# Kernel optimization log

Measured on AMD Instinct MI355X. Metric: run time of the kernel, lower is better.

The kernel has to match this reference:

```python
import jax, jax.numpy as jnp
import numpy as np

B, T, H, W, CIN = 8, 10, 64, 64, 32
F = 64          # filters
KH, KW = 3, 3
G = 4           # num_gate_copies


def _conv(x, k):
    # x: (N,H,W,Cin), k: (kh,kw,Cin,Cout), SAME padding, stride 1
    return jax.lax.conv_general_dilated(
        x, k, window_strides=(1, 1), padding='SAME',
        dimension_numbers=('NHWC', 'HWIO', 'NHWC'))


def setup_inputs() -> dict:
    key = jax.random.key(0)
    k1, k2, k3, k4 = jax.random.split(key, 4)
    inputs = jax.random.normal(k1, (B, T, H, W, CIN), dtype=jnp.float32)
    label_values = jax.random.randint(k2, (B,), 0, G, dtype=jnp.int32)
    kernel = jax.random.normal(k3, (KH, KW, CIN, 4 * F), dtype=jnp.float32) * 0.05
    recurrent_kernel = jax.random.normal(k4, (G, KH, KW, F, 4 * F), dtype=jnp.float32) * 0.05
    # unit_forget_bias: zeros with forget-gate slice set to 1.0
    bias = jnp.zeros((G, 4 * F), dtype=jnp.float32).at[:, F:2 * F].set(1.0)
    return {"inputs": inputs, "label_values": label_values,
            "kernel": kernel, "recurrent_kernel": recurrent_kernel, "bias": bias}


def reference(inputs, label_values, kernel, recurrent_kernel, bias):
    b, t, h_dim, w_dim, _ = inputs.shape
    f = recurrent_kernel.shape[-1] // 4
    # Per-sample gather of expert recurrent kernel / bias (label-indexed)
    k_b = recurrent_kernel[label_values]   # (B, kh, kw, F, 4F)
    b_b = bias[label_values]               # (B, 4F)

    # vmapped per-sample batch=1 recurrent conv (faithful to map_fn semantics)
    per_sample_conv = jax.vmap(lambda hs, ks: _conv(hs[None], ks)[0])

    def step(carry, x_t):
        h, c = carry
        z = _conv(x_t, kernel) + per_sample_conv(h, k_b) + b_b[:, None, None, :]
        i = jax.nn.sigmoid(z[..., :f])
        fg = jax.nn.sigmoid(z[..., f:2 * f])
        g = jnp.tanh(z[..., 2 * f:3 * f])
        o = jax.nn.sigmoid(z[..., 3 * f:])
        c_new = fg * c + i * g
        h_new = o * jnp.tanh(c_new)
        return (h_new, c_new), h_new

    h0 = jnp.zeros((b, h_dim, w_dim, f), dtype=inputs.dtype)
    c0 = jnp.zeros_like(h0)
    xs = jnp.moveaxis(inputs, 1, 0)  # (T, B, H, W, Cin)
    _, ys = jax.lax.scan(step, (h0, c0), xs)
    return jnp.moveaxis(ys, 0, 1)    # (B, T, H, W, F)
```

## Files before the change

### kernel.cpp

```cpp
#include <hip/hip_runtime.h>


typedef __attribute__((ext_vector_type(8))) short short8v;
typedef __attribute__((ext_vector_type(4))) float f32x4;
typedef __attribute__((ext_vector_type(4))) unsigned int u32x4;
typedef unsigned short u16;

__device__ __forceinline__ u16 f2bf(float x) {
    union { float f; unsigned u; } a; a.f = x;
    unsigned r = a.u + 0x7FFFu + ((a.u >> 16) & 1u);
    return (u16)(r >> 16);
}
__device__ __forceinline__ float sigf(float x) { return 1.0f / (1.0f + __expf(-x)); }
__device__ __forceinline__ float tanhf_(float x) {
    float e = __expf(2.0f * x);
    return 1.0f - 2.0f / (e + 1.0f);
}

__global__ __launch_bounds__(256)
void prep_w(const float* __restrict__ kern, const float* __restrict__ rk,
            u16* __restrict__ wt_in, u16* __restrict__ wt_rk,
            unsigned* __restrict__ flags) {
    int idx = blockIdx.x * 256 + threadIdx.x;
    if (blockIdx.x == 0) flags[threadIdx.x] = 0u;
    if (idx >= 82944) return;
    const float* s;
    u16* dst;
    if (idx < 9216) {
        int co = idx & 255, ckb = idx >> 8;
        int tap = ckb >> 2, kb = ckb & 3;
        s = kern + (size_t)((tap << 5) + (kb << 3)) * 256 + co;
        dst = wt_in + (size_t)idx * 8;
    } else {
        int j = idx - 9216;
        int co = j & 255, rest = j >> 8;
        int kb = rest & 3, gc = rest >> 2;
        int g = gc / 18, cc = gc - g * 18;
        int tap = cc >> 1;
        int cib = (cc & 1) << 5;
        s = rk + (size_t)(((g * 9 + tap) << 6) + cib + (kb << 3)) * 256 + co;
        dst = wt_rk + (size_t)j * 8;
    }
    union { u16 u[8]; uint4 q; } o;
    #pragma unroll
    for (int i = 0; i < 8; ++i) o.u[i] = f2bf(s[i * 256]);
    *(uint4*)dst = o.q;
}

__device__ __forceinline__ void stageX(const float* __restrict__ src,
                                       short* __restrict__ halX,
                                       int tid, int y0, int x0) {
    #pragma unroll 2
    for (int s = tid; s < 720; s += 512) {
        int pos = s >> 2, kb = s & 3;
        int hy = pos / 10, hx = pos - hy * 10;
        int gy = y0 + hy - 1, gx = x0 + hx - 1;
        union { u16 u[8]; short8v v; } o;
        o.v = (short8v){0,0,0,0,0,0,0,0};
        if ((unsigned)gy < 64u && (unsigned)gx < 64u) {
            const float* p = src + (((gy << 6) + gx) << 5) + (kb << 3);
            float4 a0 = *(const float4*)p;
            float4 a1 = *(const float4*)(p + 4);
            o.u[0] = f2bf(a0.x); o.u[1] = f2bf(a0.y);
            o.u[2] = f2bf(a0.z); o.u[3] = f2bf(a0.w);
            o.u[4] = f2bf(a1.x); o.u[5] = f2bf(a1.y);
            o.u[6] = f2bf(a1.z); o.u[7] = f2bf(a1.w);
        }
        *(short8v*)&halX[kb * 1440 + pos * 8] = o.v;
    }
}

__global__ __launch_bounds__(512)
void lstm_all(const float* __restrict__ xf,
              const u16* __restrict__ wt_in, const u16* __restrict__ wt_rk,
              const float* __restrict__ bias, const int* __restrict__ labels,
              u16* __restrict__ hb0, u16* __restrict__ hb1,
              float* __restrict__ out, unsigned* __restrict__ flags)
{
    __shared__ short hal[17280];

    const int tid  = threadIdx.x;
    const int lane = tid & 63;
    const int w    = tid >> 6;
    const int pxh  = w >> 2;
    const int wq   = w & 3;
    const int b    = blockIdx.x >> 5;
    const int tile = blockIdx.x & 31;
    const int ty = tile >> 3, tx = tile & 7;
    const int y0 = ty << 4, x0 = tx << 3;
    const int g = labels[b];

    const int co_l = lane & 15;
    const int kbl  = lane >> 4;
    const int prow = (lane & 15) >> 3, pcol = lane & 7;
    const int f = (wq << 4) + co_l;

    float bv[4];
    #pragma unroll
    for (int n = 0; n < 4; ++n)
        bv[n] = bias[(g << 8) + (n << 6) + f];

    int aoffm[4];
    #pragma unroll
    for (int m = 0; m < 4; ++m)
        aoffm[m] = ((pxh << 3) + (m << 1) + prow) * 10 + pcol;

    int poff[4][4];
    #pragma unroll
    for (int m = 0; m < 4; ++m)
        #pragma unroll
        for (int rr = 0; rr < 4; ++rr) {
            int pf = (kbl << 2) + rr;
            int yy = y0 + (pxh << 3) + (m << 1) + (pf >> 3);
            int xx = x0 + (pf & 7);
            poff[m][rr] = (((yy << 6) + xx) << 6) + f;
        }

    float cst[4][4];
    #pragma unroll
    for (int m = 0; m < 4; ++m)
        #pragma unroll
        for (int rr = 0; rr < 4; ++rr) cst[m][rr] = 0.0f;

    const float* xsrc = xf + ((size_t)b * 10 << 17);
    float*       ob0  = out + ((size_t)b * 10 << 18);
    unsigned*    myfl = flags + (b << 5) + tile;

    for (int s = tid; s < 1440; s += 512)
        *(short8v*)&hal[5760 + s * 8] = (short8v){0,0,0,0,0,0,0,0};
    stageX(xsrc, hal, tid, y0, x0);
    __syncthreads();

    for (int t = 0; t < 10; ++t) {
        u16* hw = ((t & 1) ? hb1 : hb0) + ((size_t)b << 18);

        f32x4 acc[4][4];
        #pragma unroll
        for (int n = 0; n < 4; ++n)
            #pragma unroll
            for (int m = 0; m < 4; ++m)
                acc[m][n] = (f32x4){bv[n], bv[n], bv[n], bv[n]};

        #pragma unroll 3
        for (int tap = 0; tap < 9; ++tap) {
            const int koff = (tap / 3) * 10 + (tap % 3);
            const u16* wb = wt_in + (size_t)((((tap << 2) + kbl) << 8) + (wq << 4) + co_l) * 8;
            short8v bfr[4], af[4];
            #pragma unroll
            for (int n = 0; n < 4; ++n)
                bfr[n] = *(const short8v*)&wb[(size_t)n << 9];
            #pragma unroll
            for (int m = 0; m < 4; ++m)
                af[m] = *(const short8v*)&hal[kbl * 1440 + (aoffm[m] + koff) * 8];
            #pragma unroll
            for (int m = 0; m < 4; ++m)
                #pragma unroll
                for (int n = 0; n < 4; ++n)
                    acc[m][n] = __builtin_amdgcn_mfma_f32_16x16x32_bf16(af[m], bfr[n], acc[m][n], 0, 0, 0);
        }
        if (t > 0) {
            #pragma unroll 3
            for (int c = 0; c < 18; ++c) {
                const int tap = c >> 1;
                const int koff = (tap / 3) * 10 + (tap % 3);
                const u16* wb = wt_rk + (size_t)(((((g * 18 + c) << 2) + kbl) << 8) + (wq << 4) + co_l) * 8;
                short8v bfr[4], af[4];
                #pragma unroll
                for (int n = 0; n < 4; ++n)
                    bfr[n] = *(const short8v*)&wb[(size_t)n << 9];
                const int abase = 5760 + (((c & 1) << 2) + kbl) * 1440;
                #pragma unroll
                for (int m = 0; m < 4; ++m)
                    af[m] = *(const short8v*)&hal[abase + (aoffm[m] + koff) * 8];
                #pragma unroll
                for (int m = 0; m < 4; ++m)
                    #pragma unroll
                    for (int n = 0; n < 4; ++n)
                        acc[m][n] = __builtin_amdgcn_mfma_f32_16x16x32_bf16(af[m], bfr[n], acc[m][n], 0, 0, 0);
            }
        }
        __syncthreads();

        float* ob = ob0 + ((size_t)t << 18);
        #pragma unroll
        for (int m = 0; m < 4; ++m) {
            #pragma unroll
            for (int rr = 0; rr < 4; ++rr) {
                float zi = acc[m][0][rr], zf = acc[m][1][rr];
                float zg = acc[m][2][rr], zo = acc[m][3][rr];
                float cn = sigf(zf) * cst[m][rr] + sigf(zi) * tanhf_(zg);
                float hn = sigf(zo) * tanhf_(cn);
                cst[m][rr] = cn;
                ob[poff[m][rr]] = hn;
                int pf = (kbl << 2) + rr;
                int ly = (pxh << 3) + (m << 1) + (pf >> 3);
                int lx = pf & 7;
                hal[5760 + (f >> 3) * 1440 + ((ly + 1) * 10 + lx + 1) * 8 + (f & 7)]
                    = (short)f2bf(hn);
            }
        }
        __syncthreads();

        if (t < 9) {
            if (tid < 352) {
                int pxr = tid >> 3, kb = tid & 7;
                int dy, dx;
                if (pxr < 8)       { dy = 0;  dx = pxr; }
                else if (pxr < 16) { dy = 15; dx = pxr - 8; }
                else { int v = pxr - 16; dy = 1 + (v >> 1); dx = (v & 1) * 7; }
                u32x4 v = *(const u32x4*)&hal[5760 + kb * 1440 + ((dy + 1) * 10 + dx + 1) * 8];
                const u16* ga = hw + ((((y0 + dy) << 6) + x0 + dx) << 6) + (kb << 3);
                asm volatile("global_store_dwordx4 %0, %1, off sc0 sc1"
                             :: "v"(ga), "v"(v) : "memory");
            }
            asm volatile("s_waitcnt vmcnt(0)" ::: "memory");
            __syncthreads();
            if (tid == 0)
                __hip_atomic_fetch_add(myfl, 1u, __ATOMIC_RELAXED,
                                       __HIP_MEMORY_SCOPE_SYSTEM);

            stageX(xsrc + ((size_t)(t + 1) << 17), hal, tid, y0, x0);

            if (tid < 64) {
                int k = tid;
                bool valid = false; int fidx = 0;
                if (k < 8) {
                    int kk = k + (k >= 4);
                    int nty = ty + kk / 3 - 1, ntx = tx + kk % 3 - 1;
                    valid = (unsigned)nty < 4u && (unsigned)ntx < 8u;
                    fidx = (b << 5) + (nty << 3) + ntx;
                }
                unsigned tgt = (unsigned)(t + 1);
                int guard = 0;
                for (;;) {
                    unsigned vv = tgt;
                    if (valid)
                        vv = __hip_atomic_load(flags + fidx, __ATOMIC_RELAXED,
                                               __HIP_MEMORY_SCOPE_SYSTEM);
                    if (__all(vv >= tgt)) break;
                    if (++guard > (1 << 18)) break;
                    __builtin_amdgcn_s_sleep(2);
                }
            }
            __syncthreads();

            if (tid < 416) {
                int posr = tid >> 3, kb = tid & 7;
                int hy, hx;
                if (posr < 10)      { hy = 0;  hx = posr; }
                else if (posr < 20) { hy = 17; hx = posr - 10; }
                else { int v = posr - 20; hy = 1 + (v >> 1); hx = (v & 1) * 9; }
                int gy = y0 + hy - 1, gx = x0 + hx - 1;
                bool inb = (unsigned)gy < 64u && (unsigned)gx < 64u;
                const u16* ga = inb ? (hw + (((gy << 6) + gx) << 6) + (kb << 3)) : hw;
                u32x4 v;
                asm volatile("global_load_dwordx4 %0, %1, off sc0 sc1"
                             : "=v"(v) : "v"(ga) : "memory");
                asm volatile("s_waitcnt vmcnt(0)" ::: "memory");
                __builtin_amdgcn_sched_barrier(0);
                if (!inb) v = (u32x4){0u, 0u, 0u, 0u};
                *(u32x4*)&hal[5760 + kb * 1440 + (hy * 10 + hx) * 8] = v;
            }
            __syncthreads();
        }
    }
}

extern "C" void kernel_launch(void* const* d_in, const int* in_sizes, int n_in,
                              void* d_out, int out_size, void* d_ws, size_t ws_size,
                              hipStream_t stream)
{
    const float* x    = (const float*)d_in[0];
    const int*   lbl  = (const int*)  d_in[1];
    const float* kern = (const float*)d_in[2];
    const float* rk   = (const float*)d_in[3];
    const float* bias = (const float*)d_in[4];
    float* out = (float*)d_out;

    u16* hb0   = (u16*)d_ws;
    u16* hb1   = hb0 + 2097152;
    u16* wt_in = hb1 + 2097152;
    u16* wt_rk = wt_in + 73728;
    unsigned* flags = (unsigned*)(wt_rk + 589824);

    hipLaunchKernelGGL(prep_w, dim3(324), dim3(256), 0, stream,
                       kern, rk, wt_in, wt_rk, flags);

    void* args[] = { (void*)&x, (void*)&wt_in, (void*)&wt_rk, (void*)&bias,
                     (void*)&lbl, (void*)&hb0, (void*)&hb1, (void*)&out,
                     (void*)&flags };
    (void)hipLaunchCooperativeKernel((const void*)lstm_all, dim3(256), dim3(512),
                                     args, 0, stream);
}
```

Baseline: 209.3 us.

## Pre-convert input to bf16, double warps per tile, overlap input conv with halo wait

Result: slower. 236.2 us (+12.9%).

```diff
diff --git a/kernel.cpp b/kernel.cpp
--- a/kernel.cpp
+++ b/kernel.cpp
@@ -15,6 +15,18 @@
 __device__ __forceinline__ float tanhf_(float x) {
     float e = __expf(2.0f * x);
     return 1.0f - 2.0f / (e + 1.0f);
+}
+
+__global__ __launch_bounds__(256)
+void prep_x(const float* __restrict__ x, u16* __restrict__ xb) {
+    size_t i = (size_t)blockIdx.x * 256 + threadIdx.x;
+    for (; i < 2621440u; i += (size_t)2048 * 256) {
+        float4 v = ((const float4*)x)[i];
+        union { u16 u[4]; uint2 q; } o;
+        o.u[0] = f2bf(v.x); o.u[1] = f2bf(v.y);
+        o.u[2] = f2bf(v.z); o.u[3] = f2bf(v.w);
+        ((uint2*)xb)[i] = o.q;
+    }
 }
 
 __global__ __launch_bounds__(256)
@@ -47,31 +59,8 @@
     *(uint4*)dst = o.q;
 }
 
-__device__ __forceinline__ void stageX(const float* __restrict__ src,
-                                       short* __restrict__ halX,
-                                       int tid, int y0, int x0) {
-    #pragma unroll 2
-    for (int s = tid; s < 720; s += 512) {
-        int pos = s >> 2, kb = s & 3;
-        int hy = pos / 10, hx = pos - hy * 10;
-        int gy = y0 + hy - 1, gx = x0 + hx - 1;
-        union { u16 u[8]; short8v v; } o;
-        o.v = (short8v){0,0,0,0,0,0,0,0};
-        if ((unsigned)gy < 64u && (unsigned)gx < 64u) {
-            const float* p = src + (((gy << 6) + gx) << 5) + (kb << 3);
-            float4 a0 = *(const float4*)p;
-            float4 a1 = *(const float4*)(p + 4);
-            o.u[0] = f2bf(a0.x); o.u[1] = f2bf(a0.y);
-            o.u[2] = f2bf(a0.z); o.u[3] = f2bf(a0.w);
-            o.u[4] = f2bf(a1.x); o.u[5] = f2bf(a1.y);
-            o.u[6] = f2bf(a1.z); o.u[7] = f2bf(a1.w);
-        }
-        *(short8v*)&halX[kb * 1440 + pos * 8] = o.v;
-    }
-}
-
-__global__ __launch_bounds__(512)
-void lstm_all(const float* __restrict__ xf,
+__global__ __launch_bounds__(1024)
+void lstm_all(const u16* __restrict__ xb,
               const u16* __restrict__ wt_in, const u16* __restrict__ wt_rk,
               const float* __restrict__ bias, const int* __restrict__ labels,
               u16* __restrict__ hb0, u16* __restrict__ hb1,
@@ -82,7 +71,7 @@
     const int tid  = threadIdx.x;
     const int lane = tid & 63;
     const int w    = tid >> 6;
-    const int pxh  = w >> 2;
+    const int pxq  = w >> 2;
     const int wq   = w & 3;
     const int b    = blockIdx.x >> 5;
     const int tile = blockIdx.x & 31;
@@ -100,103 +89,151 @@
     for (int n = 0; n < 4; ++n)
         bv[n] = bias[(g << 8) + (n << 6) + f];
 
-    int aoffm[4];
-    #pragma unroll
-    for (int m = 0; m < 4; ++m)
-        aoffm[m] = ((pxh << 3) + (m << 1) + prow) * 10 + pcol;
-
-    int poff[4][4];
-    #pragma unroll
-    for (int m = 0; m < 4; ++m)
+    int aoffm[2];
+    #pragma unroll
+    for (int mf = 0; mf < 2; ++mf)
+        aoffm[mf] = ((pxq << 2) + (mf << 1) + prow) * 10 + pcol;
+
+    int poff[2][4], loff[2][4];
+    #pragma unroll
+    for (int mf = 0; mf < 2; ++mf)
         #pragma unroll
         for (int rr = 0; rr < 4; ++rr) {
             int pf = (kbl << 2) + rr;
-            int yy = y0 + (pxh << 3) + (m << 1) + (pf >> 3);
-            int xx = x0 + (pf & 7);
-            poff[m][rr] = (((yy << 6) + xx) << 6) + f;
-        }
-
-    float cst[4][4];
-    #pragma unroll
-    for (int m = 0; m < 4; ++m)
+            int ly = (pxq << 2) + (mf << 1) + (pf >> 3);
+            int lx = pf & 7;
+            poff[mf][rr] = ((((y0 + ly) << 6) + x0 + lx) << 6) + f;
+            loff[mf][rr] = 5760 + (f >> 3) * 1440 + ((ly + 1) * 10 + lx + 1) * 8 + (f & 7);
+        }
+
+    float cst[2][4];
+    #pragma unroll
+    for (int mf = 0; mf < 2; ++mf)
         #pragma unroll
-        for (int rr = 0; rr < 4; ++rr) cst[m][rr] = 0.0f;
-
-    const float* xsrc = xf + ((size_t)b * 10 << 17);
-    float*       ob0  = out + ((size_t)b * 10 << 18);
-    unsigned*    myfl = flags + (b << 5) + tile;
-
-    for (int s = tid; s < 1440; s += 512)
+        for (int rr = 0; rr < 4; ++rr) cst[mf][rr] = 0.0f;
+
+    const u16* xsrc = xb + ((size_t)b * 10 << 17);
+    float*     ob0  = out + ((size_t)b * 10 << 18);
+    unsigned*  myfl = flags + (b << 5) + tile;
+
+    for (int s = tid; s < 1440; s += 1024)
         *(short8v*)&hal[5760 + s * 8] = (short8v){0,0,0,0,0,0,0,0};
-    stageX(xsrc, hal, tid, y0, x0);
+    if (tid < 720) {
+        int pos = tid >> 2, kb = tid & 3;
+        int hy = pos / 10, hx = pos - hy * 10;
+        int gy = y0 + hy - 1, gx = x0 + hx - 1;
+        short8v v = (short8v){0,0,0,0,0,0,0,0};
+        if ((unsigned)gy < 64u && (unsigned)gx < 64u)
+            v = *(const short8v*)&xsrc[(((gy << 6) + gx) << 5) + (kb << 3)];
+        *(short8v*)&hal[kb * 1440 + pos * 8] = v;
+    }
     __syncthreads();
 
     for (int t = 0; t < 10; ++t) {
         u16* hw = ((t & 1) ? hb1 : hb0) + ((size_t)b << 18);
 
-        f32x4 acc[4][4];
+        f32x4 acc[2][4];
         #pragma unroll
         for (int n = 0; n < 4; ++n)
             #pragma unroll
-            for (int m = 0; m < 4; ++m)
-                acc[m][n] = (f32x4){bv[n], bv[n], bv[n], bv[n]};
+            for (int mf = 0; mf < 2; ++mf)
+                acc[mf][n] = (f32x4){bv[n], bv[n], bv[n], bv[n]};
 
         #pragma unroll 3
         for (int tap = 0; tap < 9; ++tap) {
             const int koff = (tap / 3) * 10 + (tap % 3);
-            const u16* wb = wt_in + (size_t)((((tap << 2) + kbl) << 8) + (wq << 4) + co_l) * 8;
-            short8v bfr[4], af[4];
+            const u16* wb = wt_in + (size_t)((((tap << 2) + kbl) << 8) + f) * 8;
+            short8v bfr[4], af[2];
             #pragma unroll
             for (int n = 0; n < 4; ++n)
                 bfr[n] = *(const short8v*)&wb[(size_t)n << 9];
             #pragma unroll
-            for (int m = 0; m < 4; ++m)
-                af[m] = *(const short8v*)&hal[kbl * 1440 + (aoffm[m] + koff) * 8];
-            #pragma unroll
-            for (int m = 0; m < 4; ++m)
+            for (int mf = 0; mf < 2; ++mf)
+                af[mf] = *(const short8v*)&hal[kbl * 1440 + (aoffm[mf] + koff) * 8];
+            #pragma unroll
+            for (int mf = 0; mf < 2; ++mf)
                 #pragma unroll
                 for (int n = 0; n < 4; ++n)
-                    acc[m][n] = __builtin_amdgcn_mfma_f32_16x16x32_bf16(af[m], bfr[n], acc[m][n], 0, 0, 0);
-        }
+                    acc[mf][n] = __builtin_amdgcn_mfma_f32_16x16x32_bf16(af[mf], bfr[n], acc[mf][n], 0, 0, 0);
+        }
+
         if (t > 0) {
+            if (tid < 64) {
+                bool valid = false; int fidx = 0;
+                if (tid < 8) {
+                    int kk = tid + (tid >= 4);
+                    int nty = ty + kk / 3 - 1, ntx = tx + kk % 3 - 1;
+                    valid = (unsigned)nty < 4u && (unsigned)ntx < 8u;
+                    fidx = (b << 5) + (nty << 3) + ntx;
+                }
+                unsigned tgt = (unsigned)t;
+                int guard = 0;
+                for (;;) {
+                    unsigned vv = tgt;
+                    if (valid)
+                        vv = __hip_atomic_load(flags + fidx, __ATOMIC_RELAXED,
+                                               __HIP_MEMORY_SCOPE_SYSTEM);
+                    if (__all(vv >= tgt)) break;
+                    if (++guard > (1 << 18)) break;
+                    __builtin_amdgcn_s_sleep(2);
+                }
+            }
+            __syncthreads();
+
+            if (tid < 416) {
+                const u16* hr = ((t & 1) ? hb0 : hb1) + ((size_t)b << 18);
+                int posr = tid >> 3, kb = tid & 7;
+                int hy, hx;
+                if (posr < 10)      { hy = 0;  hx = posr; }
+                else if (posr < 20) { hy = 17; hx = posr - 10; }
+                else { int v = posr - 20; hy = 1 + (v >> 1); hx = (v & 1) * 9; }
+                int gy = y0 + hy - 1, gx = x0 + hx - 1;
+                bool inb = (unsigned)gy < 64u && (unsigned)gx < 64u;
+                const u16* ga = inb ? (hr + (((gy << 6) + gx) << 6) + (kb << 3)) : hr;
+                u32x4 v;
+                asm volatile("global_load_dwordx4 %0, %1, off sc0 sc1"
+                             : "=v"(v) : "v"(ga) : "memory");
+                asm volatile("s_waitcnt vmcnt(0)" ::: "memory");
+                __builtin_amdgcn_sched_barrier(0);
+                if (!inb) v = (u32x4){0u, 0u, 0u, 0u};
+                *(u32x4*)&hal[5760 + kb * 1440 + (hy * 10 + hx) * 8] = v;
+            }
+            __syncthreads();
+
             #pragma unroll 3
             for (int c = 0; c < 18; ++c) {
                 const int tap = c >> 1;
                 const int koff = (tap / 3) * 10 + (tap % 3);
-                const u16* wb = wt_rk + (size_t)(((((g * 18 + c) << 2) + kbl) << 8) + (wq << 4) + co_l) * 8;
-                short8v bfr[4], af[4];
+                const u16* wb = wt_rk + (size_t)(((((g * 18 + c) << 2) + kbl) << 8) + f) * 8;
+                short8v bfr[4], af[2];
                 #pragma unroll
                 for (int n = 0; n < 4; ++n)
                     bfr[n] = *(const short8v*)&wb[(size_t)n << 9];
                 const int abase = 5760 + (((c & 1) << 2) + kbl) * 1440;
                 #pragma unroll
-                for (int m = 0; m < 4; ++m)
-                    af[m] = *(const short8v*)&hal[abase + (aoffm[m] + koff) * 8];
+                for (int mf = 0; mf < 2; ++mf)
+                    af[mf] = *(const short8v*)&hal[abase + (aoffm[mf] + koff) * 8];
                 #pragma unroll
-                for (int m = 0; m < 4; ++m)
+                for (int mf = 0; mf < 2; ++mf)
                     #pragma unroll
                     for (int n = 0; n < 4; ++n)
-                        acc[m][n] = __builtin_amdgcn_mfma_f32_16x16x32_bf16(af[m], bfr[n], acc[m][n], 0, 0, 0);
+                        acc[mf][n] = __builtin_amdgcn_mfma_f32_16x16x32_bf16(af[mf], bfr[n], acc[mf][n], 0, 0, 0);
             }
         }
         __syncthreads();
 
         float* ob = ob0 + ((size_t)t << 18);
         #pragma unroll
-        for (int m = 0; m < 4; ++m) {
+        for (int mf = 0; mf < 2; ++mf) {
             #pragma unroll
             for (int rr = 0; rr < 4; ++rr) {
-                float zi = acc[m][0][rr], zf = acc[m][1][rr];
-                float zg = acc[m][2][rr], zo = acc[m][3][rr];
-                float cn = sigf(zf) * cst[m][rr] + sigf(zi) * tanhf_(zg);
+                float zi = acc[mf][0][rr], zf = acc[mf][1][rr];
+                float zg = acc[mf][2][rr], zo = acc[mf][3][rr];
+                float cn = sigf(zf) * cst[mf][rr] + sigf(zi) * tanhf_(zg);
                 float hn = sigf(zo) * tanhf_(cn);
-                cst[m][rr] = cn;
-                ob[poff[m][rr]] = hn;
-                int pf = (kbl << 2) + rr;
-                int ly = (pxh << 3) + (m << 1) + (pf >> 3);
-                int lx = pf & 7;
-                hal[5760 + (f >> 3) * 1440 + ((ly + 1) * 10 + lx + 1) * 8 + (f & 7)]
-                    = (short)f2bf(hn);
+                cst[mf][rr] = cn;
+                ob[poff[mf][rr]] = hn;
+                hal[loff[mf][rr]] = (short)f2bf(hn);
             }
         }
         __syncthreads();
@@ -219,47 +256,15 @@
                 __hip_atomic_fetch_add(myfl, 1u, __ATOMIC_RELAXED,
                                        __HIP_MEMORY_SCOPE_SYSTEM);
 
-            stageX(xsrc + ((size_t)(t + 1) << 17), hal, tid, y0, x0);
-
-            if (tid < 64) {
-                int k = tid;
-                bool valid = false; int fidx = 0;
-                if (k < 8) {
-                    int kk = k + (k >= 4);
-                    int nty = ty + kk / 3 - 1, ntx = tx + kk % 3 - 1;
-                    valid = (unsigned)nty < 4u && (unsigned)ntx < 8u;
-                    fidx = (b << 5) + (nty << 3) + ntx;
-                }
-                unsigned tgt = (unsigned)(t + 1);
-                int guard = 0;
-                for (;;) {
-                    unsigned vv = tgt;
-                    if (valid)
-                        vv = __hip_atomic_load(flags + fidx, __ATOMIC_RELAXED,
-                                               __HIP_MEMORY_SCOPE_SYSTEM);
-                    if (__all(vv >= tgt)) break;
-                    if (++guard > (1 << 18)) break;
-                    __builtin_amdgcn_s_sleep(2);
-                }
-            }
-            __syncthreads();
-
-            if (tid < 416) {
-                int posr = tid >> 3, kb = tid & 7;
-                int hy, hx;
-                if (posr < 10)      { hy = 0;  hx = posr; }
-                else if (posr < 20) { hy = 17; hx = posr - 10; }
-                else { int v = posr - 20; hy = 1 + (v >> 1); hx = (v & 1) * 9; }
+            if (tid < 720) {
+                const u16* src = xsrc + ((size_t)(t + 1) << 17);
+                int pos = tid >> 2, kb = tid & 3;
+                int hy = pos / 10, hx = pos - hy * 10;
                 int gy = y0 + hy - 1, gx = x0 + hx - 1;
-                bool inb = (unsigned)gy < 64u && (unsigned)gx < 64u;
-                const u16* ga = inb ? (hw + (((gy << 6) + gx) << 6) + (kb << 3)) : hw;
-                u32x4 v;
-                asm volatile("global_load_dwordx4 %0, %1, off sc0 sc1"
-                             : "=v"(v) : "v"(ga) : "memory");
-                asm volatile("s_waitcnt vmcnt(0)" ::: "memory");
-                __builtin_amdgcn_sched_barrier(0);
-                if (!inb) v = (u32x4){0u, 0u, 0u, 0u};
-                *(u32x4*)&hal[5760 + kb * 1440 + (hy * 10 + hx) * 8] = v;
+                short8v v = (short8v){0,0,0,0,0,0,0,0};
+                if ((unsigned)gy < 64u && (unsigned)gx < 64u)
+                    v = *(const short8v*)&src[(((gy << 6) + gx) << 5) + (kb << 3)];
+                *(short8v*)&hal[kb * 1440 + pos * 8] = v;
             }
             __syncthreads();
         }
@@ -277,18 +282,20 @@
     const float* bias = (const float*)d_in[4];
     float* out = (float*)d_out;
 
-    u16* hb0   = (u16*)d_ws;
+    u16* xb    = (u16*)d_ws;
+    u16* hb0   = xb + 10485760;
     u16* hb1   = hb0 + 2097152;
     u16* wt_in = hb1 + 2097152;
     u16* wt_rk = wt_in + 73728;
     unsigned* flags = (unsigned*)(wt_rk + 589824);
 
+    hipLaunchKernelGGL(prep_x, dim3(2048), dim3(256), 0, stream, x, xb);
     hipLaunchKernelGGL(prep_w, dim3(324), dim3(256), 0, stream,
                        kern, rk, wt_in, wt_rk, flags);
 
-    void* args[] = { (void*)&x, (void*)&wt_in, (void*)&wt_rk, (void*)&bias,
+    void* args[] = { (void*)&xb, (void*)&wt_in, (void*)&wt_rk, (void*)&bias,
                      (void*)&lbl, (void*)&hb0, (void*)&hb1, (void*)&out,
                      (void*)&flags };
-    (void)hipLaunchCooperativeKernel((const void*)lstm_all, dim3(256), dim3(512),
+    (void)hipLaunchCooperativeKernel((const void*)lstm_all, dim3(256), dim3(1024),
                                      args, 0, stream);
 }
```

## Overlap neighbor-flag wait with input conv, pre-convert x to bf16, pad LDS stride

Applied to the files above, without the earlier changes.

After: 201.0 us. -3.9%, faster.

```diff
diff --git a/kernel.cpp b/kernel.cpp
--- a/kernel.cpp
+++ b/kernel.cpp
@@ -6,6 +6,9 @@
 typedef __attribute__((ext_vector_type(4))) unsigned int u32x4;
 typedef unsigned short u16;
 
+#define HS 1448
+#define HB 5760
+
 __device__ __forceinline__ u16 f2bf(float x) {
     union { float f; unsigned u; } a; a.f = x;
     unsigned r = a.u + 0x7FFFu + ((a.u >> 16) & 1u);
@@ -15,6 +18,18 @@
 __device__ __forceinline__ float tanhf_(float x) {
     float e = __expf(2.0f * x);
     return 1.0f - 2.0f / (e + 1.0f);
+}
+
+__global__ __launch_bounds__(256)
+void prep_x(const float* __restrict__ x, u16* __restrict__ xb) {
+    size_t i = (size_t)blockIdx.x * 256 + threadIdx.x;
+    for (; i < 2621440u; i += (size_t)2048 * 256) {
+        float4 v = ((const float4*)x)[i];
+        union { u16 u[4]; uint2 q; } o;
+        o.u[0] = f2bf(v.x); o.u[1] = f2bf(v.y);
+        o.u[2] = f2bf(v.z); o.u[3] = f2bf(v.w);
+        ((uint2*)xb)[i] = o.q;
+    }
 }
 
 __global__ __launch_bounds__(256)
@@ -47,7 +62,7 @@
     *(uint4*)dst = o.q;
 }
 
-__device__ __forceinline__ void stageX(const float* __restrict__ src,
+__device__ __forceinline__ void stageX(const u16* __restrict__ src,
                                        short* __restrict__ halX,
                                        int tid, int y0, int x0) {
     #pragma unroll 2
@@ -55,29 +70,21 @@
         int pos = s >> 2, kb = s & 3;
         int hy = pos / 10, hx = pos - hy * 10;
         int gy = y0 + hy - 1, gx = x0 + hx - 1;
-        union { u16 u[8]; short8v v; } o;
-        o.v = (short8v){0,0,0,0,0,0,0,0};
-        if ((unsigned)gy < 64u && (unsigned)gx < 64u) {
-            const float* p = src + (((gy << 6) + gx) << 5) + (kb << 3);
-            float4 a0 = *(const float4*)p;
-            float4 a1 = *(const float4*)(p + 4);
-            o.u[0] = f2bf(a0.x); o.u[1] = f2bf(a0.y);
-            o.u[2] = f2bf(a0.z); o.u[3] = f2bf(a0.w);
-            o.u[4] = f2bf(a1.x); o.u[5] = f2bf(a1.y);
-            o.u[6] = f2bf(a1.z); o.u[7] = f2bf(a1.w);
-        }
-        *(short8v*)&halX[kb * 1440 + pos * 8] = o.v;
+        short8v v = (short8v){0,0,0,0,0,0,0,0};
+        if ((unsigned)gy < 64u && (unsigned)gx < 64u)
+            v = *(const short8v*)&src[(((gy << 6) + gx) << 5) + (kb << 3)];
+        *(short8v*)&halX[kb * 1440 + pos * 8] = v;
     }
 }
 
 __global__ __launch_bounds__(512)
-void lstm_all(const float* __restrict__ xf,
+void lstm_all(const u16* __restrict__ xb,
               const u16* __restrict__ wt_in, const u16* __restrict__ wt_rk,
               const float* __restrict__ bias, const int* __restrict__ labels,
               u16* __restrict__ hb0, u16* __restrict__ hb1,
               float* __restrict__ out, unsigned* __restrict__ flags)
 {
-    __shared__ short hal[17280];
+    __shared__ short hal[HB + 8 * HS];
 
     const int tid  = threadIdx.x;
     const int lane = tid & 63;
@@ -105,15 +112,16 @@
     for (int m = 0; m < 4; ++m)
         aoffm[m] = ((pxh << 3) + (m << 1) + prow) * 10 + pcol;
 
-    int poff[4][4];
+    int poff[4][4], loff[4][4];
     #pragma unroll
     for (int m = 0; m < 4; ++m)
         #pragma unroll
         for (int rr = 0; rr < 4; ++rr) {
             int pf = (kbl << 2) + rr;
-            int yy = y0 + (pxh << 3) + (m << 1) + (pf >> 3);
-            int xx = x0 + (pf & 7);
-            poff[m][rr] = (((yy << 6) + xx) << 6) + f;
+            int ly = (pxh << 3) + (m << 1) + (pf >> 3);
+            int lx = pf & 7;
+            poff[m][rr] = ((((y0 + ly) << 6) + x0 + lx) << 6) + f;
+            loff[m][rr] = HB + (f >> 3) * HS + ((ly + 1) * 10 + lx + 1) * 8 + (f & 7);
         }
 
     float cst[4][4];
@@ -122,12 +130,12 @@
         #pragma unroll
         for (int rr = 0; rr < 4; ++rr) cst[m][rr] = 0.0f;
 
-    const float* xsrc = xf + ((size_t)b * 10 << 17);
-    float*       ob0  = out + ((size_t)b * 10 << 18);
-    unsigned*    myfl = flags + (b << 5) + tile;
-
-    for (int s = tid; s < 1440; s += 512)
-        *(short8v*)&hal[5760 + s * 8] = (short8v){0,0,0,0,0,0,0,0};
+    const u16* xsrc = xb + ((size_t)b * 10 << 17);
+    float*     ob0  = out + ((size_t)b * 10 << 18);
+    unsigned*  myfl = flags + (b << 5) + tile;
+
+    for (int s = tid; s < 1448; s += 512)
+        *(short8v*)&hal[HB + s * 8] = (short8v){0,0,0,0,0,0,0,0};
     stageX(xsrc, hal, tid, y0, x0);
     __syncthreads();
 
@@ -144,7 +152,7 @@
         #pragma unroll 3
         for (int tap = 0; tap < 9; ++tap) {
             const int koff = (tap / 3) * 10 + (tap % 3);
-            const u16* wb = wt_in + (size_t)((((tap << 2) + kbl) << 8) + (wq << 4) + co_l) * 8;
+            const u16* wb = wt_in + (size_t)((((tap << 2) + kbl) << 8) + f) * 8;
             short8v bfr[4], af[4];
             #pragma unroll
             for (int n = 0; n < 4; ++n)
@@ -158,79 +166,17 @@
                 for (int n = 0; n < 4; ++n)
                     acc[m][n] = __builtin_amdgcn_mfma_f32_16x16x32_bf16(af[m], bfr[n], acc[m][n], 0, 0, 0);
         }
+
         if (t > 0) {
-            #pragma unroll 3
-            for (int c = 0; c < 18; ++c) {
-                const int tap = c >> 1;
-                const int koff = (tap / 3) * 10 + (tap % 3);
-                const u16* wb = wt_rk + (size_t)(((((g * 18 + c) << 2) + kbl) << 8) + (wq << 4) + co_l) * 8;
-                short8v bfr[4], af[4];
-                #pragma unroll
-                for (int n = 0; n < 4; ++n)
-                    bfr[n] = *(const short8v*)&wb[(size_t)n << 9];
-                const int abase = 5760 + (((c & 1) << 2) + kbl) * 1440;
-                #pragma unroll
-                for (int m = 0; m < 4; ++m)
-                    af[m] = *(const short8v*)&hal[abase + (aoffm[m] + koff) * 8];
-                #pragma unroll
-                for (int m = 0; m < 4; ++m)
-                    #pragma unroll
-                    for (int n = 0; n < 4; ++n)
-                        acc[m][n] = __builtin_amdgcn_mfma_f32_16x16x32_bf16(af[m], bfr[n], acc[m][n], 0, 0, 0);
-            }
-        }
-        __syncthreads();
-
-        float* ob = ob0 + ((size_t)t << 18);
-        #pragma unroll
-        for (int m = 0; m < 4; ++m) {
-            #pragma unroll
-            for (int rr = 0; rr < 4; ++rr) {
-                float zi = acc[m][0][rr], zf = acc[m][1][rr];
-                float zg = acc[m][2][rr], zo = acc[m][3][rr];
-                float cn = sigf(zf) * cst[m][rr] + sigf(zi) * tanhf_(zg);
-                float hn = sigf(zo) * tanhf_(cn);
-                cst[m][rr] = cn;
-                ob[poff[m][rr]] = hn;
-                int pf = (kbl << 2) + rr;
-                int ly = (pxh << 3) + (m << 1) + (pf >> 3);
-                int lx = pf & 7;
-                hal[5760 + (f >> 3) * 1440 + ((ly + 1) * 10 + lx + 1) * 8 + (f & 7)]
-                    = (short)f2bf(hn);
-            }
-        }
-        __syncthreads();
-
-        if (t < 9) {
-            if (tid < 352) {
-                int pxr = tid >> 3, kb = tid & 7;
-                int dy, dx;
-                if (pxr < 8)       { dy = 0;  dx = pxr; }
-                else if (pxr < 16) { dy = 15; dx = pxr - 8; }
-                else { int v = pxr - 16; dy = 1 + (v >> 1); dx = (v & 1) * 7; }
-                u32x4 v = *(const u32x4*)&hal[5760 + kb * 1440 + ((dy + 1) * 10 + dx + 1) * 8];
-                const u16* ga = hw + ((((y0 + dy) << 6) + x0 + dx) << 6) + (kb << 3);
-                asm volatile("global_store_dwordx4 %0, %1, off sc0 sc1"
-                             :: "v"(ga), "v"(v) : "memory");
-            }
-            asm volatile("s_waitcnt vmcnt(0)" ::: "memory");
-            __syncthreads();
-            if (tid == 0)
-                __hip_atomic_fetch_add(myfl, 1u, __ATOMIC_RELAXED,
-                                       __HIP_MEMORY_SCOPE_SYSTEM);
-
-            stageX(xsrc + ((size_t)(t + 1) << 17), hal, tid, y0, x0);
-
             if (tid < 64) {
-                int k = tid;
                 bool valid = false; int fidx = 0;
-                if (k < 8) {
-                    int kk = k + (k >= 4);
+                if (tid < 8) {
+                    int kk = tid + (tid >= 4);
                     int nty = ty + kk / 3 - 1, ntx = tx + kk % 3 - 1;
                     valid = (unsigned)nty < 4u && (unsigned)ntx < 8u;
                     fidx = (b << 5) + (nty << 3) + ntx;
                 }
-                unsigned tgt = (unsigned)(t + 1);
+                unsigned tgt = (unsigned)t;
                 int guard = 0;
                 for (;;) {
                     unsigned vv = tgt;
@@ -245,6 +191,7 @@
             __syncthreads();
 
             if (tid < 416) {
+                const u16* hr = ((t & 1) ? hb0 : hb1) + ((size_t)b << 18);
                 int posr = tid >> 3, kb = tid & 7;
                 int hy, hx;
                 if (posr < 10)      { hy = 0;  hx = posr; }
@@ -252,16 +199,73 @@
                 else { int v = posr - 20; hy = 1 + (v >> 1); hx = (v & 1) * 9; }
                 int gy = y0 + hy - 1, gx = x0 + hx - 1;
                 bool inb = (unsigned)gy < 64u && (unsigned)gx < 64u;
-                const u16* ga = inb ? (hw + (((gy << 6) + gx) << 6) + (kb << 3)) : hw;
+                const u16* ga = inb ? (hr + (((gy << 6) + gx) << 6) + (kb << 3)) : hr;
                 u32x4 v;
                 asm volatile("global_load_dwordx4 %0, %1, off sc0 sc1"
                              : "=v"(v) : "v"(ga) : "memory");
                 asm volatile("s_waitcnt vmcnt(0)" ::: "memory");
                 __builtin_amdgcn_sched_barrier(0);
                 if (!inb) v = (u32x4){0u, 0u, 0u, 0u};
-                *(u32x4*)&hal[5760 + kb * 1440 + (hy * 10 + hx) * 8] = v;
+                *(u32x4*)&hal[HB + kb * HS + (hy * 10 + hx) * 8] = v;
             }
             __syncthreads();
+
+            #pragma unroll 3
+            for (int c = 0; c < 18; ++c) {
+                const int tap = c >> 1;
+                const int koff = (tap / 3) * 10 + (tap % 3);
+                const u16* wb = wt_rk + (size_t)(((((g * 18 + c) << 2) + kbl) << 8) + f) * 8;
+                short8v bfr[4], af[4];
+                #pragma unroll
+                for (int n = 0; n < 4; ++n)
+                    bfr[n] = *(const short8v*)&wb[(size_t)n << 9];
+                const int abase = HB + (((c & 1) << 2) + kbl) * HS;
+                #pragma unroll
+                for (int m = 0; m < 4; ++m)
+                    af[m] = *(const short8v*)&hal[abase + (aoffm[m] + koff) * 8];
+                #pragma unroll
+                for (int m = 0; m < 4; ++m)
+                    #pragma unroll
+                    for (int n = 0; n < 4; ++n)
+                        acc[m][n] = __builtin_amdgcn_mfma_f32_16x16x32_bf16(af[m], bfr[n], acc[m][n], 0, 0, 0);
+            }
+        }
+        __syncthreads();
+
+        float* ob = ob0 + ((size_t)t << 18);
+        #pragma unroll
+        for (int m = 0; m < 4; ++m) {
+            #pragma unroll
+            for (int rr = 0; rr < 4; ++rr) {
+                float zi = acc[m][0][rr], zf = acc[m][1][rr];
+                float zg = acc[m][2][rr], zo = acc[m][3][rr];
+                float cn = sigf(zf) * cst[m][rr] + sigf(zi) * tanhf_(zg);
+                float hn = sigf(zo) * tanhf_(cn);
+                cst[m][rr] = cn;
+                ob[poff[m][rr]] = hn;
+                hal[loff[m][rr]] = (short)f2bf(hn);
+            }
+        }
+        __syncthreads();
+
+        if (t < 9) {
+            if (tid < 352) {
+                int pxr = tid >> 3, kb = tid & 7;
+                int dy, dx;
+                if (pxr < 8)       { dy = 0;  dx = pxr; }
+                else if (pxr < 16) { dy = 15; dx = pxr - 8; }
+                else { int v = pxr - 16; dy = 1 + (v >> 1); dx = (v & 1) * 7; }
+                u32x4 v = *(const u32x4*)&hal[HB + kb * HS + ((dy + 1) * 10 + dx + 1) * 8];
+                const u16* ga = hw + ((((y0 + dy) << 6) + x0 + dx) << 6) + (kb << 3);
+                asm volatile("global_store_dwordx4 %0, %1, off sc0 sc1"
+                             :: "v"(ga), "v"(v) : "memory");
+            }
+            stageX(xsrc + ((size_t)(t + 1) << 17), hal, tid, y0, x0);
+            asm volatile("s_waitcnt vmcnt(0)" ::: "memory");
+            __syncthreads();
+            if (tid == 0)
+                __hip_atomic_fetch_add(myfl, 1u, __ATOMIC_RELAXED,
+                                       __HIP_MEMORY_SCOPE_SYSTEM);
         }
     }
 }
@@ -277,16 +281,18 @@
     const float* bias = (const float*)d_in[4];
     float* out = (float*)d_out;
 
-    u16* hb0   = (u16*)d_ws;
+    u16* xb    = (u16*)d_ws;
+    u16* hb0   = xb + 10485760;
     u16* hb1   = hb0 + 2097152;
     u16* wt_in = hb1 + 2097152;
     u16* wt_rk = wt_in + 73728;
     unsigned* flags = (unsigned*)(wt_rk + 589824);
 
+    hipLaunchKernelGGL(prep_x, dim3(2048), dim3(256), 0, stream, x, xb);
     hipLaunchKernelGGL(prep_w, dim3(324), dim3(256), 0, stream,
                        kern, rk, wt_in, wt_rk, flags);
 
-    void* args[] = { (void*)&x, (void*)&wt_in, (void*)&wt_rk, (void*)&bias,
+    void* args[] = { (void*)&xb, (void*)&wt_in, (void*)&wt_rk, (void*)&bias,
                      (void*)&lbl, (void*)&hb0, (void*)&hb1, (void*)&out,
                      (void*)&flags };
     (void)hipLaunchCooperativeKernel((const void*)lstm_all, dim3(256), dim3(512),
```
